# Kernel optimization log

Hardware: AMD Instinct MI355X
Metric: run time of the kernel (lower is better)

## Reference

```python
import jax, jax.numpy as jnp
import numpy as np

LOG2 = 13          # log2_num_embeddings -> K = 8192 codes
TEMP = 1.0         # forward default temperature
BN_EPS = 1e-5

def _codebook_bits():
    ints = jnp.arange(2 ** LOG2)
    bits = (ints[:, None] & (1 << jnp.arange(LOG2 - 1, -1, -1))) > 0
    return bits.astype(jnp.float32)  # [K, LOG2]

def _bn_relu(x, g, b):
    # training-mode BatchNorm1d (biased batch stats) + ReLU
    m = x.mean(axis=0)
    v = x.var(axis=0)
    return jax.nn.relu(g * (x - m) * jax.lax.rsqrt(v + BN_EPS) + b)

def _embed_mlp(bits, w_in, b_in, wh, bh, gammas, betas, w_out, b_out):
    x = _bn_relu(bits @ w_in + b_in, gammas[0], betas[0])
    for i in range(wh.shape[0]):  # 4 hidden blocks (condition_layer=6)
        x = _bn_relu(x @ wh[i] + bh[i], gammas[i + 1], betas[i + 1])
    return x @ w_out + b_out  # [K, vq_dim]

def _normalize(x):
    return x / (jnp.linalg.norm(x, axis=-1, keepdims=True) + 1e-6)

def setup_inputs() -> dict:
    key = jax.random.key(0)
    ks = jax.random.split(key, 8)
    B, L, D, VQ, HID = 4, 2048, 512, 64, 1024
    s = 0.02
    return {
        "h_in": jax.random.normal(ks[0], (B, L, D), jnp.float32),
        "attn_mask": jax.random.randint(ks[1], (B, L), 0, 2, jnp.int32),
        "proj_w": jax.random.normal(ks[2], (D, VQ), jnp.float32) * s,
        "proj_b": jnp.zeros((VQ,), jnp.float32),
        "inv_w": jax.random.normal(ks[3], (VQ, D), jnp.float32) * s,
        "inv_b": jnp.zeros((D,), jnp.float32),
        "mlp_w_in": jax.random.normal(ks[4], (LOG2, HID), jnp.float32) * s,
        "mlp_b_in": jnp.zeros((HID,), jnp.float32),
        "mlp_wh": jax.random.normal(ks[5], (4, HID, HID), jnp.float32) * s,
        "mlp_bh": jnp.zeros((4, HID), jnp.float32),
        "mlp_gammas": jnp.ones((5, HID), jnp.float32),
        "mlp_betas": jnp.zeros((5, HID), jnp.float32),
        "mlp_w_out": jax.random.normal(ks[6], (HID, VQ), jnp.float32) * s,
        "mlp_b_out": jnp.zeros((VQ,), jnp.float32),
    }

def reference(h_in, attn_mask, proj_w, proj_b, inv_w, inv_b,
              mlp_w_in, mlp_b_in, mlp_wh, mlp_bh, mlp_gammas, mlp_betas,
              mlp_w_out, mlp_b_out):
    # project + codebook MLP
    h = h_in @ proj_w + proj_b                                  # [B,L,VQ]
    embed = _embed_mlp(_codebook_bits(), mlp_w_in, mlp_b_in, mlp_wh, mlp_bh,
                       mlp_gammas, mlp_betas, mlp_w_out, mlp_b_out)  # [K,VQ]
    h = _normalize(h)
    embed = _normalize(embed)

    B, L, D = h.shape
    h_flat = h.reshape(B * L, D)
    mask = attn_mask.reshape(-1)                                # int {0,1}
    maskf = mask.astype(h.dtype)

    # attention: distances = -2*(alpha-1)*sg(H C^T) - 2*H C^T ; A = softmax(-d)
    hc = h_flat @ embed.T                                       # [BL,K]
    alpha = 1.0 / TEMP
    distances = -2.0 * (alpha - 1.0) * jax.lax.stop_gradient(hc) - 2.0 * hc
    A = jax.nn.softmax(-distances, axis=1)

    # codebook repulsion loss: max off-diagonal similarity
    mat = embed @ embed.T                                       # [K,K]
    K = mat.shape[0]
    idx = jnp.arange(K)
    mat = mat.at[idx, idx].set(-1.0)
    vq_loss = mat.max(axis=-1).mean()

    # multinomial sample from A == categorical over logits -distances
    code = jax.random.categorical(jax.random.key(1), -distances, axis=-1)
    onehot = jax.nn.one_hot(code, K, dtype=A.dtype)
    # c = onehot - A ; A2 = A + sg(c)  (straight-through one-hot)
    A2 = A + jax.lax.stop_gradient(onehot - A)
    h_vq = h_flat + A2 @ embed - jax.lax.stop_gradient(h_flat)  # [BL,VQ]

    # scatter back into zeros at masked-out positions, then inverse proj
    quantized = (h_vq * maskf[:, None]).reshape(B, L, D)
    quantized = quantized @ inv_w + inv_b                       # [B,L,512]
    vq_code = (code * mask.astype(code.dtype)).reshape(B, L)
    return quantized, vq_code, vq_loss
```

## Files before the change

### kernel.cpp

```cpp
#include <hip/hip_runtime.h>
#include <hip/hip_bf16.h>
#include <stdint.h>

#define HID 1024

__device__ __forceinline__ uint32_t rotl32(uint32_t x, int r) {
  return (x << r) | (x >> (32 - r));
}

__device__ __forceinline__ uint2 threefry2x32_01(uint32_t x0, uint32_t x1) {
  const uint32_t k0 = 0u, k1 = 1u;
  const uint32_t k2 = k0 ^ k1 ^ 0x1BD11BDAu;
  x0 += k0; x1 += k1;
#define TF_R(r) { x0 += x1; x1 = rotl32(x1, r); x1 ^= x0; }
  TF_R(13) TF_R(15) TF_R(26) TF_R(6)
  x0 += k1; x1 += k2 + 1u;
  TF_R(17) TF_R(29) TF_R(16) TF_R(24)
  x0 += k2; x1 += k0 + 2u;
  TF_R(13) TF_R(15) TF_R(26) TF_R(6)
  x0 += k0; x1 += k1 + 3u;
  TF_R(17) TF_R(29) TF_R(16) TF_R(24)
  x0 += k1; x1 += k2 + 4u;
  TF_R(13) TF_R(15) TF_R(26) TF_R(6)
  x0 += k2; x1 += k0 + 5u;
#undef TF_R
  return make_uint2(x0, x1);
}

__device__ __noinline__ float gumbel_at(uint32_t flat) {
  uint2 y = threefry2x32_01(0u, flat);
  uint32_t b = y.x ^ y.y;
  float f = __uint_as_float((b >> 9) | 0x3f800000u) - 1.0f;
  float u = fmaxf(f, 1.17549435e-38f);
  float w = -(float)log((double)u);
  float o = (float)log((double)w);
  return -o;
}

__device__ __forceinline__ float f4c(const float4& v, int i) {
  return i == 0 ? v.x : (i == 1 ? v.y : (i == 2 ? v.z : v.w));
}

template<int BM, int BN_, int BK, int TM, int TN, bool FUSE_BN>
__global__ void __launch_bounds__(256, 4) gemm_bn_relu(
    const float* __restrict__ A, const float* __restrict__ B,
    const float* __restrict__ bias, const float* __restrict__ bna,
    const float* __restrict__ bnc, float* __restrict__ C,
    int M, int N, int K)
{
  __shared__ __align__(16) float As[BK][BM + 4];
  __shared__ __align__(16) float Bs[BK][BN_];
  const int t = threadIdx.x;
  const int n0 = blockIdx.x * BN_;
  const int m0 = blockIdx.y * BM;
  const int tn = t % (BN_ / TN);
  const int tm = t / (BN_ / TN);

  float acc[TM][TN];
#pragma unroll
  for (int i = 0; i < TM; ++i)
#pragma unroll
    for (int j = 0; j < TN; ++j) acc[i][j] = 0.f;

  for (int k0 = 0; k0 < K; k0 += BK) {
    __syncthreads();
#pragma unroll
    for (int p = 0; p < BM * BK / 1024; ++p) {
      int f = t + p * 256;
      int kq = f % (BK / 4);
      int m = f / (BK / 4);
      float4 v = *(const float4*)(A + (size_t)(m0 + m) * K + (k0 + kq * 4));
      if constexpr (FUSE_BN) {
        float4 a4 = *(const float4*)(bna + k0 + kq * 4);
        float4 c4 = *(const float4*)(bnc + k0 + kq * 4);
        v.x = fmaxf(fmaf(v.x, a4.x, c4.x), 0.f);
        v.y = fmaxf(fmaf(v.y, a4.y, c4.y), 0.f);
        v.z = fmaxf(fmaf(v.z, a4.z, c4.z), 0.f);
        v.w = fmaxf(fmaf(v.w, a4.w, c4.w), 0.f);
      }
      As[kq * 4 + 0][m] = v.x;
      As[kq * 4 + 1][m] = v.y;
      As[kq * 4 + 2][m] = v.z;
      As[kq * 4 + 3][m] = v.w;
    }
#pragma unroll
    for (int p = 0; p < BK * BN_ / 1024; ++p) {
      int f = t + p * 256;
      int n4 = f % (BN_ / 4);
      int k = f / (BN_ / 4);
      *(float4*)&Bs[k][n4 * 4] =
          *(const float4*)(B + (size_t)(k0 + k) * N + (n0 + n4 * 4));
    }
    __syncthreads();
#pragma unroll 4
    for (int kk = 0; kk < BK; ++kk) {
      float a[TM], b[TN];
      {
        float4 q0 = *(const float4*)&As[kk][tm * 4];
        a[0] = q0.x; a[1] = q0.y; a[2] = q0.z; a[3] = q0.w;
        if constexpr (TM == 8) {
          float4 q1 = *(const float4*)&As[kk][tm * 4 + BM / 2];
          a[4] = q1.x; a[5] = q1.y; a[6] = q1.z; a[7] = q1.w;
        }
        float4 r0 = *(const float4*)&Bs[kk][tn * 4];
        b[0] = r0.x; b[1] = r0.y; b[2] = r0.z; b[3] = r0.w;
        if constexpr (TN == 8) {
          float4 r1 = *(const float4*)&Bs[kk][tn * 4 + BN_ / 2];
          b[4] = r1.x; b[5] = r1.y; b[6] = r1.z; b[7] = r1.w;
        }
      }
#pragma unroll
      for (int i = 0; i < TM; ++i)
#pragma unroll
        for (int j = 0; j < TN; ++j)
          acc[i][j] = fmaf(a[i], b[j], acc[i][j]);
    }
  }
#pragma unroll
  for (int i = 0; i < TM; ++i) {
    int m = (i < 4) ? (tm * 4 + i) : (tm * 4 + BM / 2 + (i - 4));
#pragma unroll
    for (int jq = 0; jq < TN / 4; ++jq) {
      int n = tn * 4 + jq * (BN_ / 2);
      float4 bv = *(const float4*)(bias + n0 + n);
      float4 o;
      o.x = acc[i][jq * 4 + 0] + bv.x;
      o.y = acc[i][jq * 4 + 1] + bv.y;
      o.z = acc[i][jq * 4 + 2] + bv.z;
      o.w = acc[i][jq * 4 + 3] + bv.w;
      *(float4*)(C + (size_t)(m0 + m) * N + (n0 + n)) = o;
    }
  }
}

__global__ void __launch_bounds__(256) embed_bits_in(
    const float* __restrict__ w_in, const float* __restrict__ b_in,
    float* __restrict__ X)
{
  int k = blockIdx.x;
  int c = threadIdx.x * 4;
  float4 acc = *(const float4*)(b_in + c);
#pragma unroll
  for (int j = 0; j < 13; ++j) {
    if (k & (1 << (12 - j))) {
      float4 w = *(const float4*)(w_in + j * HID + c);
      acc.x += w.x; acc.y += w.y; acc.z += w.z; acc.w += w.w;
    }
  }
  *(float4*)(X + (size_t)k * HID + c) = acc;
}

__global__ void __launch_bounds__(256) bn_stats_partial(
    const float* __restrict__ X, float* __restrict__ part)
{
  int cb = blockIdx.x, rb = blockIdx.y;
  int t = threadIdx.x;
  int cl = t & 31, rs = t >> 5;
  int c = cb * 32 + cl;
  int r0 = rb * 256 + rs * 32;
  float s = 0.f, sq = 0.f;
  const float* p = X + (size_t)r0 * HID + c;
  for (int i = 0; i < 32; ++i) {
    float v = p[(size_t)i * HID];
    s += v;
    sq = fmaf(v, v, sq);
  }
  __shared__ float rs_[8][32], rq_[8][32];
  rs_[rs][cl] = s;
  rq_[rs][cl] = sq;
  __syncthreads();
  if (t < 32) {
    float S = 0.f, Q = 0.f;
    for (int i = 0; i < 8; ++i) { S += rs_[i][t]; Q += rq_[i][t]; }
    size_t o = ((size_t)rb * HID + cb * 32 + t) * 2;
    part[o] = S;
    part[o + 1] = Q;
  }
}

__global__ void __launch_bounds__(256) bn_finalize(
    const float* __restrict__ part, const float* __restrict__ gamma,
    const float* __restrict__ beta, float* __restrict__ bna,
    float* __restrict__ bnc)
{
  int c = blockIdx.x * 256 + threadIdx.x;
  double S = 0.0, Q = 0.0;
  for (int rb = 0; rb < 32; ++rb) {
    size_t o = ((size_t)rb * HID + c) * 2;
    S += (double)part[o];
    Q += (double)part[o + 1];
  }
  double mean = S / 8192.0;
  double var = Q / 8192.0 - mean * mean;
  float r = (float)(1.0 / sqrt(var + 1e-5));
  float a = gamma[c] * r;
  bna[c] = a;
  bnc[c] = fmaf(-(float)mean, a, beta[c]);
}

__global__ void __launch_bounds__(64) row_normalize64(
    const float* __restrict__ in, float* __restrict__ out)
{
  int r = blockIdx.x, t = threadIdx.x;
  float v = in[(size_t)r * 64 + t];
  float ss = v * v;
  for (int m = 32; m >= 1; m >>= 1) ss += __shfl_xor(ss, m);
  float inv = 1.f / (sqrtf(ss) + 1e-6f);
  out[(size_t)r * 64 + t] = v * inv;
}

template<bool GUM>
__global__ void __launch_bounds__(256, 2) score_kernel(
    const float* __restrict__ Arows, const float* __restrict__ eN,
    float* __restrict__ pval, int* __restrict__ pidx)
{
  __shared__ __align__(16) float Ed[64][256];
  __shared__ __align__(16) float Hs[32][64];
  const int t = threadIdx.x;
  const int i0 = (blockIdx.x >> 1) * 32;
  const int kh = blockIdx.x & 1;
  for (int f = t; f < 512; f += 256) {
    int lr = f >> 4, dq = (f & 15) << 2;
    *(float4*)&Hs[lr][dq] = *(const float4*)(Arows + (size_t)(i0 + lr) * 64 + dq);
  }
  const int kg = t & 31;
  const int rg = t >> 5;
  float best[4];
  int bidx[4];
#pragma unroll
  for (int r = 0; r < 4; ++r) { best[r] = -3.4e38f; bidx[r] = 0; }

  for (int tile = 0; tile < 16; ++tile) {
    const int kb = kh * 4096 + tile * 256;
    __syncthreads();
#pragma unroll
    for (int p = 0; p < 16; ++p) {
      int kk = p * 16 + (t >> 4);
      int dq = (t & 15) << 2;
      float4 v = *(const float4*)(eN + (size_t)(kb + kk) * 64 + dq);
      Ed[dq + 0][kk ^ ((dq + 0) & 28)] = v.x;
      Ed[dq + 1][kk ^ ((dq + 1) & 28)] = v.y;
      Ed[dq + 2][kk ^ ((dq + 2) & 28)] = v.z;
      Ed[dq + 3][kk ^ ((dq + 3) & 28)] = v.w;
    }
    __syncthreads();
    float acc[4][8];
#pragma unroll
    for (int r = 0; r < 4; ++r)
#pragma unroll
      for (int q = 0; q < 8; ++q) acc[r][q] = 0.f;

#pragma unroll 2
    for (int dq = 0; dq < 64; dq += 4) {
      float4 hq[4];
      hq[0] = *(const float4*)&Hs[rg * 4 + 0][dq];
      hq[1] = *(const float4*)&Hs[rg * 4 + 1][dq];
      hq[2] = *(const float4*)&Hs[rg * 4 + 2][dq];
      hq[3] = *(const float4*)&Hs[rg * 4 + 3][dq];
#pragma unroll
      for (int dd = 0; dd < 4; ++dd) {
        const int d = dq + dd;
        const int s = d & 28;
        const float4 ea = *(const float4*)&Ed[d][(kg * 4) ^ s];
        const float4 eb = *(const float4*)&Ed[d][(128 + kg * 4) ^ s];
#pragma unroll
        for (int r = 0; r < 4; ++r) {
          const float hv = f4c(hq[r], dd);
          acc[r][0] = fmaf(hv, ea.x, acc[r][0]);
          acc[r][1] = fmaf(hv, ea.y, acc[r][1]);
          acc[r][2] = fmaf(hv, ea.z, acc[r][2]);
          acc[r][3] = fmaf(hv, ea.w, acc[r][3]);
          acc[r][4] = fmaf(hv, eb.x, acc[r][4]);
          acc[r][5] = fmaf(hv, eb.y, acc[r][5]);
          acc[r][6] = fmaf(hv, eb.z, acc[r][6]);
          acc[r][7] = fmaf(hv, eb.w, acc[r][7]);
        }
      }
    }
#pragma unroll
    for (int r = 0; r < 4; ++r) {
      const uint32_t grow = (uint32_t)(i0 + rg * 4 + r);
#pragma unroll
      for (int q = 0; q < 8; ++q) {
        const int kl = (q < 4) ? (kg * 4 + q) : (128 + kg * 4 + (q - 4));
        const int kgl = kb + kl;
        if constexpr (GUM) {
          float g = gumbel_at((grow << 13) | (uint32_t)kgl);
          float z = 2.f * acc[r][q] + g;
          if (z > best[r]) { best[r] = z; bidx[r] = kgl; }
        } else {
          float z = (kgl == (int)grow) ? -1.0f : acc[r][q];
          if (z > best[r]) best[r] = z;
        }
      }
    }
  }
#pragma unroll
  for (int r = 0; r < 4; ++r) {
    float bv = best[r];
    int bi = bidx[r];
    for (int m = 16; m >= 1; m >>= 1) {
      float ov = __shfl_xor(bv, m);
      int oi = __shfl_xor(bi, m);
      if (ov > bv || (GUM && ov == bv && oi < bi)) { bv = ov; bi = oi; }
    }
    if ((t & 31) == 0) {
      int grow = i0 + rg * 4 + r;
      pval[grow * 2 + kh] = bv;
      if constexpr (GUM) pidx[grow * 2 + kh] = bi;
    }
  }
}

__global__ void __launch_bounds__(256) combine_kernel(
    const float* __restrict__ pval, const int* __restrict__ pidx,
    const float* __restrict__ pmax, const int* __restrict__ mask,
    int* __restrict__ codes, float* __restrict__ out_code,
    float* __restrict__ losspart)
{
  int r = blockIdx.x * 256 + threadIdx.x;
  float v0 = pval[r * 2], v1 = pval[r * 2 + 1];
  int code = (v1 > v0) ? pidx[r * 2 + 1] : pidx[r * 2];
  codes[r] = code;
  out_code[r] = (mask[r] != 0) ? (float)code : 0.f;
  float m = fmaxf(pmax[r * 2], pmax[r * 2 + 1]);
  __shared__ float red[256];
  red[threadIdx.x] = m;
  __syncthreads();
  for (int s = 128; s >= 1; s >>= 1) {
    if (threadIdx.x < s) red[threadIdx.x] += red[threadIdx.x + s];
    __syncthreads();
  }
  if (threadIdx.x == 0) losspart[blockIdx.x] = red[0];
}

__global__ void __launch_bounds__(64) loss_final(
    const float* __restrict__ losspart, float* __restrict__ out)
{
  float s = (threadIdx.x < 32) ? losspart[threadIdx.x] : 0.f;
  for (int m = 32; m >= 1; m >>= 1) s += __shfl_xor(s, m);
  if (threadIdx.x == 0) out[0] = s * (1.0f / 8192.0f);
}

__global__ void __launch_bounds__(256, 2) final_proj(
    const float* __restrict__ eN, const int* __restrict__ codes,
    const int* __restrict__ mask, const float* __restrict__ inv_w,
    const float* __restrict__ inv_b, float* __restrict__ out)
{
  __shared__ __align__(16) float Ws[64][128];
  __shared__ __align__(16) float Es[32][64];
  const int t = threadIdx.x;
  const int c0 = blockIdx.x * 128;
  const int r0 = blockIdx.y * 32;
  for (int f = t; f < 512; f += 256) {
    int lr = f >> 4, dq = (f & 15) << 2;
    int grow = r0 + lr;
    float4 v = make_float4(0.f, 0.f, 0.f, 0.f);
    if (mask[grow] != 0)
      v = *(const float4*)(eN + (size_t)codes[grow] * 64 + dq);
    *(float4*)&Es[lr][dq] = v;
  }
  for (int f = t; f < 2048; f += 256) {
    int n4 = f & 31, j = f >> 5;
    *(float4*)&Ws[j][n4 * 4] =
        *(const float4*)(inv_w + (size_t)j * 512 + c0 + n4 * 4);
  }
  __syncthreads();
  const int tx = t & 31, ty = t >> 5;
  float acc[4][4];
#pragma unroll
  for (int r = 0; r < 4; ++r)
#pragma unroll
    for (int j = 0; j < 4; ++j) acc[r][j] = 0.f;
#pragma unroll 4
  for (int j = 0; j < 64; ++j) {
    float4 wv = *(const float4*)&Ws[j][tx * 4];
#pragma unroll
    for (int r = 0; r < 4; ++r) {
      float e = Es[ty * 4 + r][j];
      acc[r][0] = fmaf(e, wv.x, acc[r][0]);
      acc[r][1] = fmaf(e, wv.y, acc[r][1]);
      acc[r][2] = fmaf(e, wv.z, acc[r][2]);
      acc[r][3] = fmaf(e, wv.w, acc[r][3]);
    }
  }
  float4 bv = *(const float4*)(inv_b + c0 + tx * 4);
#pragma unroll
  for (int r = 0; r < 4; ++r) {
    float4 o;
    o.x = acc[r][0] + bv.x;
    o.y = acc[r][1] + bv.y;
    o.z = acc[r][2] + bv.z;
    o.w = acc[r][3] + bv.w;
    *(float4*)(out + (size_t)(r0 + ty * 4 + r) * 512 + c0 + tx * 4) = o;
  }
}

extern "C" void kernel_launch(void* const* d_in, const int* in_sizes, int n_in,
                              void* d_out, int out_size, void* d_ws, size_t ws_size,
                              hipStream_t stream) {
  (void)in_sizes; (void)n_in; (void)out_size; (void)ws_size;
  const float* h_in   = (const float*)d_in[0];
  const int*   mask   = (const int*)d_in[1];
  const float* proj_w = (const float*)d_in[2];
  const float* proj_b = (const float*)d_in[3];
  const float* inv_w  = (const float*)d_in[4];
  const float* inv_b  = (const float*)d_in[5];
  const float* w_in   = (const float*)d_in[6];
  const float* b_in   = (const float*)d_in[7];
  const float* wh     = (const float*)d_in[8];
  const float* bh     = (const float*)d_in[9];
  const float* gam    = (const float*)d_in[10];
  const float* bet    = (const float*)d_in[11];
  const float* w_out  = (const float*)d_in[12];
  const float* b_out  = (const float*)d_in[13];

  float* ws = (float*)d_ws;
  float* XA = ws;
  float* XB = ws + 8388608;
  float* scr = ws + 16777216;
  float* stats   = scr;
  float* pval    = scr;
  int*   pidx    = (int*)(scr + 16384);
  float* pmax    = scr + 32768;
  int*   codes   = (int*)(scr + 49152);
  float* losspart = scr + 57344;
  float* bna = ws + 16842752;
  float* bnc = bna + 1024;
  float* h_norm = ws + 16844800;
  float* e_norm = h_norm + 524288;

  float* out = (float*)d_out;
  float* out_q = out;
  float* out_code = out + 4194304;
  float* out_loss = out + 4202496;

  gemm_bn_relu<64, 64, 32, 4, 4, false><<<dim3(1, 128), 256, 0, stream>>>(
      h_in, proj_w, proj_b, nullptr, nullptr, XB, 8192, 64, 512);
  row_normalize64<<<8192, 64, 0, stream>>>(XB, h_norm);

  embed_bits_in<<<8192, 256, 0, stream>>>(w_in, b_in, XA);
  float* Xcur = XA;
  float* Xnext = XB;
  for (int l = 0; l < 5; ++l) {
    bn_stats_partial<<<dim3(32, 32), 256, 0, stream>>>(Xcur, stats);
    bn_finalize<<<4, 256, 0, stream>>>(stats, gam + l * 1024, bet + l * 1024, bna, bnc);
    if (l < 4) {
      gemm_bn_relu<128, 128, 32, 8, 8, true><<<dim3(8, 64), 256, 0, stream>>>(
          Xcur, wh + (size_t)l * 1024 * 1024, bh + l * 1024, bna, bnc, Xnext,
          8192, 1024, 1024);
      float* tmp = Xcur; Xcur = Xnext; Xnext = tmp;
    } else {
      gemm_bn_relu<64, 64, 32, 4, 4, true><<<dim3(1, 128), 256, 0, stream>>>(
          Xcur, w_out, b_out, bna, bnc, Xnext, 8192, 64, 1024);
    }
  }
  row_normalize64<<<8192, 64, 0, stream>>>(Xnext, e_norm);

  score_kernel<true><<<512, 256, 0, stream>>>(h_norm, e_norm, pval, pidx);
  score_kernel<false><<<512, 256, 0, stream>>>(e_norm, e_norm, pmax, nullptr);

  combine_kernel<<<32, 256, 0, stream>>>(pval, pidx, pmax, mask, codes, out_code, losspart);
  loss_final<<<1, 64, 0, stream>>>(losspart, out_loss);
  final_proj<<<dim3(4, 256), 256, 0, stream>>>(e_norm, codes, mask, inv_w, inv_b, out_q);
}
```

Before: 1.830 ms.

## Use fast float log for Gumbel noise with top-2 exact rescoring

Replaces the per-element double-precision log Gumbel computation in the sampling score kernel with fast single-precision __logf. The kernel now tracks the top-2 candidates per row and recomputes the exact double-precision Gumbel only for the winner, and for the runner-up when it lies within a small margin, so the chosen code matches the exact path. This removes the heavy per-element double-precision log cost. In exchange it adds register pressure from the extra candidate tracking and a more complex warp reduction. Exactness depends on the fast-log error staying below the margin.

```diff
diff --git a/kernel.cpp b/kernel.cpp
--- a/kernel.cpp
+++ b/kernel.cpp
@@ -27,11 +27,21 @@
   return make_uint2(x0, x1);
 }
 
-__device__ __noinline__ float gumbel_at(uint32_t flat) {
+__device__ __forceinline__ float uni_at(uint32_t flat) {
   uint2 y = threefry2x32_01(0u, flat);
   uint32_t b = y.x ^ y.y;
   float f = __uint_as_float((b >> 9) | 0x3f800000u) - 1.0f;
-  float u = fmaxf(f, 1.17549435e-38f);
+  return fmaxf(f, 1.17549435e-38f);
+}
+
+__device__ __forceinline__ float gumbel_fast(uint32_t flat) {
+  float u = uni_at(flat);
+  float w = -__logf(u);
+  return -__logf(w);
+}
+
+__device__ __noinline__ float gumbel_exact(uint32_t flat) {
+  float u = uni_at(flat);
   float w = -(float)log((double)u);
   float o = (float)log((double)w);
   return -o;
@@ -39,6 +49,10 @@
 
 __device__ __forceinline__ float f4c(const float4& v, int i) {
   return i == 0 ? v.x : (i == 1 ? v.y : (i == 2 ? v.z : v.w));
+}
+
+__device__ __forceinline__ bool rank_above(float av, int ai, float bv, int bi) {
+  return av > bv || (av == bv && ai < bi);
 }
 
 template<int BM, int BN_, int BK, int TM, int TN, bool FUSE_BN>
@@ -225,10 +239,12 @@
   }
   const int kg = t & 31;
   const int rg = t >> 5;
-  float best[4];
-  int bidx[4];
-#pragma unroll
-  for (int r = 0; r < 4; ++r) { best[r] = -3.4e38f; bidx[r] = 0; }
+  float b1[4], b2[4];
+  int i1[4], i2[4];
+#pragma unroll
+  for (int r = 0; r < 4; ++r) {
+    b1[r] = -3.4e38f; b2[r] = -3.4e38f; i1[r] = 0; i2[r] = 0;
+  }
 
   for (int tile = 0; tile < 16; ++tile) {
     const int kb = kh * 4096 + tile * 256;
@@ -285,29 +301,63 @@
         const int kl = (q < 4) ? (kg * 4 + q) : (128 + kg * 4 + (q - 4));
         const int kgl = kb + kl;
         if constexpr (GUM) {
-          float g = gumbel_at((grow << 13) | (uint32_t)kgl);
+          float g = gumbel_fast((grow << 13) | (uint32_t)kgl);
           float z = 2.f * acc[r][q] + g;
-          if (z > best[r]) { best[r] = z; bidx[r] = kgl; }
+          if (z > b1[r]) {
+            b2[r] = b1[r]; i2[r] = i1[r];
+            b1[r] = z; i1[r] = kgl;
+          } else if (z > b2[r]) {
+            b2[r] = z; i2[r] = kgl;
+          }
         } else {
           float z = (kgl == (int)grow) ? -1.0f : acc[r][q];
-          if (z > best[r]) best[r] = z;
+          if (z > b1[r]) b1[r] = z;
         }
       }
     }
   }
 #pragma unroll
   for (int r = 0; r < 4; ++r) {
-    float bv = best[r];
-    int bi = bidx[r];
-    for (int m = 16; m >= 1; m >>= 1) {
-      float ov = __shfl_xor(bv, m);
-      int oi = __shfl_xor(bi, m);
-      if (ov > bv || (GUM && ov == bv && oi < bi)) { bv = ov; bi = oi; }
-    }
-    if ((t & 31) == 0) {
-      int grow = i0 + rg * 4 + r;
-      pval[grow * 2 + kh] = bv;
-      if constexpr (GUM) pidx[grow * 2 + kh] = bi;
+    if constexpr (GUM) {
+      float v1 = b1[r], v2 = b2[r];
+      int j1 = i1[r], j2 = i2[r];
+      for (int m = 16; m >= 1; m >>= 1) {
+        float o1 = __shfl_xor(v1, m), o2 = __shfl_xor(v2, m);
+        int p1 = __shfl_xor(j1, m), p2 = __shfl_xor(j2, m);
+        if (rank_above(o1, p1, v1, j1)) {
+          float nv2; int nj2;
+          if (rank_above(v1, j1, o2, p2)) { nv2 = v1; nj2 = j1; }
+          else { nv2 = o2; nj2 = p2; }
+          v1 = o1; j1 = p1; v2 = nv2; j2 = nj2;
+        } else {
+          if (rank_above(o1, p1, v2, j2)) { v2 = o1; j2 = p1; }
+        }
+      }
+      if ((t & 31) == 0) {
+        const uint32_t grow = (uint32_t)(i0 + rg * 4 + r);
+        float g1f = gumbel_fast((grow << 13) | (uint32_t)j1);
+        float g1e = gumbel_exact((grow << 13) | (uint32_t)j1);
+        float z1 = v1 - g1f + g1e;
+        int win = j1;
+        if (v1 - v2 <= 1e-3f) {
+          float g2f = gumbel_fast((grow << 13) | (uint32_t)j2);
+          float g2e = gumbel_exact((grow << 13) | (uint32_t)j2);
+          float z2 = v2 - g2f + g2e;
+          if (rank_above(z2, j2, z1, win)) { z1 = z2; win = j2; }
+        }
+        pval[grow * 2 + kh] = z1;
+        pidx[grow * 2 + kh] = win;
+      }
+    } else {
+      float bv = b1[r];
+      for (int m = 16; m >= 1; m >>= 1) {
+        float ov = __shfl_xor(bv, m);
+        if (ov > bv) bv = ov;
+      }
+      if ((t & 31) == 0) {
+        int grow = i0 + rg * 4 + r;
+        pval[grow * 2 + kh] = bv;
+      }
     }
   }
 }
```

New measurement: 1.595 ms. 1.15x faster.
